# Kernel tuning notes

Hardware: AMD Instinct MI355X
Metric: run time of the kernel (lower is better)

## Reference

```python
import jax, jax.numpy as jnp
import numpy as np

B, SQ, SK, D, DV = 16, 2048, 2048, 128, 128
NUM_HEADS = 2
DROPOUT_P = 0.1
SCALE_FACTOR = 1.0 / (DROPOUT_P * NUM_HEADS)  # = 5.0; scores are divided by this


def setup_inputs() -> dict:
    key = jax.random.key(0)
    k1, k2, k3, k4 = jax.random.split(key, 4)
    x1 = jax.random.normal(k1, (B, SQ, D), dtype=jnp.float32)
    x2 = jax.random.normal(k2, (B, SK, D), dtype=jnp.float32)
    x3 = jax.random.normal(k3, (B, SK, DV), dtype=jnp.float32)
    # deterministic dropout keep-mask (True -> keep), keep prob = 1 - p
    drop_mask = jax.random.bernoulli(k4, 1.0 - DROPOUT_P, (B, SQ, SK))
    return {"x1": x1, "x2": x2, "x3": x3, "drop_mask": drop_mask}


def reference(x1, x2, x3, drop_mask):
    # v1 = x1 @ x2^T : [B, Sq, Sk]
    scores = jnp.einsum("bqd,bkd->bqk", x1, x2)
    # v2 = v1 / scale_factor (scale_factor = 1/(p*heads) = 5 -> multiply by 0.2)
    scores = scores * (1.0 / SCALE_FACTOR)
    probs = jax.nn.softmax(scores, axis=-1)
    # dropout with inverted scaling 1/(1-p)
    keep_scale = 1.0 / (1.0 - DROPOUT_P)
    probs = jnp.where(drop_mask, probs * keep_scale, 0.0)
    # output = probs @ x3 : [B, Sq, Dv]
    return jnp.einsum("bqk,bkv->bqv", probs, x3)
```

## Files before the change

kernel.cpp:

```cpp
#include <hip/hip_runtime.h>
#include <stdint.h>


#define B_   16
#define SQ_  2048
#define SK_  2048
#define D_   128
#define DV_  128
#define BK   64
#define NT   (SK_ / BK)

typedef short  s16x8 __attribute__((ext_vector_type(8)));
typedef float  f32x4 __attribute__((ext_vector_type(4)));
typedef unsigned int u32x4 __attribute__((ext_vector_type(4)));
typedef unsigned short u16;
typedef unsigned int   u32;

__device__ __forceinline__ u32 pk2(float a, float b) {
    u32 r;
    asm("v_cvt_pk_bf16_f32 %0, %1, %2" : "=v"(r) : "v"(a), "v"(b));
    return r;
}
__device__ __forceinline__ u16 f2bf(float f) { return (u16)pk2(f, 0.0f); }

__device__ __forceinline__ void gload16(u16* lds, const u16* g) {
    __builtin_amdgcn_global_load_lds((const __attribute__((address_space(1))) u32*)g,
                                     (__attribute__((address_space(3))) u32*)lds,
                                     16, 0, 0);
}

__global__ __launch_bounds__(256)
void prep_k(const float* __restrict__ Kg, u16* __restrict__ Kz)
{
    int g   = blockIdx.x * 256 + threadIdx.x;
    int b   = g >> 15;
    int rem = g & 32767;
    int k   = rem >> 4;
    int grp = rem & 15;
    const float* src = Kg + ((size_t)b * SK_ + k) * D_ + grp * 8;
    float4 x = *(const float4*)(src);
    float4 y = *(const float4*)(src + 4);
    u32x4 w = { pk2(x.x, x.y), pk2(x.z, x.w), pk2(y.x, y.y), pk2(y.z, y.w) };
    int c = (grp * 8) ^ ((k & 7) << 3);
    *(u32x4*)(&Kz[((size_t)b * SK_ + k) * D_ + c]) = w;
}

__global__ __launch_bounds__(256)
void prep_v(const float* __restrict__ Vg, u16* __restrict__ Vz)
{
    int g  = blockIdx.x * 256 + threadIdx.x;
    int kg = g & 7;
    int dv = (g >> 3) & 127;
    int kt = (g >> 10) & 31;
    int b  = g >> 15;
    const float* src = Vg + ((size_t)b * SK_ + kt * 64 + kg * 8) * DV_ + dv;
    float v[8];
    #pragma unroll
    for (int jj = 0; jj < 8; ++jj) v[jj] = src[(size_t)jj * DV_];
    u32x4 w = { pk2(v[0], v[1]), pk2(v[2], v[3]), pk2(v[4], v[5]), pk2(v[6], v[7]) };
    int c = (kg * 8) ^ ((dv & 7) << 3);
    *(u32x4*)(&Vz[(((size_t)b * 32 + kt) * 128 + dv) * 64 + c]) = w;
}

#define BODY(IT, MC, MN)                                                      \
  {                                                                           \
    __syncthreads();              \
    {                                                                         \
      const u16* Kt = Kz + kvbase + (size_t)(IT) * 8192;                      \
      const u16* Vt = Vz + kvbase + (size_t)(IT) * 8192;                      \
      _Pragma("unroll")                                                       \
      for (int i = 0; i < 4; ++i) {                                           \
        int c16 = (wave * 4 + i) * 512;                                       \
        gload16(&Ks[c16], &Kt[c16 + lane * 8]);                               \
        gload16(&Vs[c16], &Vt[c16 + lane * 8]);                               \
      }                                                                       \
    }                                                                         \
    __syncthreads();           \
    if ((IT) + 1 < NT) {                                                      \
      _Pragma("unroll")                                                       \
      for (int t = 0; t < 2; ++t)                                             \
        _Pragma("unroll")                                                     \
        for (int r = 0; r < 4; ++r)                                           \
          MN[t][r] = Mg[mbase + (size_t)r * SK_ + ((IT) + 1) * 64 + t * 16];  \
    }                                                                         \
    f32x4 s[2];                                                               \
    s[0] = (f32x4){0.f, 0.f, 0.f, 0.f};                                       \
    s[1] = (f32x4){0.f, 0.f, 0.f, 0.f};                                       \
    __builtin_amdgcn_s_setprio(1);                                            \
    _Pragma("unroll")                                                         \
    for (int kb = 0; kb < 4; ++kb) {                                          \
      _Pragma("unroll")                                                       \
      for (int t = 0; t < 2; ++t) {                                           \
        int kcol = kh * 32 + t * 16 + n16;                                    \
        int coff = (kb * 32 + quad * 8) ^ ((kcol & 7) << 3);                  \
        s16x8 bK = *(const s16x8*)(&Ks[kcol * 128 + coff]);                   \
        s[t] = __builtin_amdgcn_mfma_f32_16x16x32_bf16(aQ[kb], bK, s[t], 0, 0, 0); \
      }                                                                       \
    }                                                                         \
    __builtin_amdgcn_s_setprio(0);                                            \
    _Pragma("unroll")                                                         \
    for (int t = 0; t < 2; ++t)                                               \
      _Pragma("unroll")                                                       \
      for (int r = 0; r < 4; ++r) {                                           \
        float p = __expf(fmaf(s[t][r], 0.2f, -12.0f));                        \
        l_part[r] += p;                                   \
        float pv = MC[t][r] ? p : 0.f;                           \
        Ps[wave * 640 + (quad * 4 + r) * 40 + t * 16 + n16] = f2bf(pv);       \
      }                                                                       \
    s16x8 aP = *(const s16x8*)(&Ps[wave * 640 + n16 * 40 + quad * 8]);        \
    __builtin_amdgcn_s_setprio(1);                                            \
    _Pragma("unroll")                                                         \
    for (int nt = 0; nt < 8; ++nt) {                                          \
      int dv = nt * 16 + n16;                                                 \
      int coff = (kh * 32 + quad * 8) ^ ((dv & 7) << 3);                      \
      s16x8 bV = *(const s16x8*)(&Vs[dv * 64 + coff]);                        \
      o[nt] = __builtin_amdgcn_mfma_f32_16x16x32_bf16(aP, bV, o[nt], 0, 0, 0); \
    }                                                                         \
    __builtin_amdgcn_s_setprio(0);                                            \
  }

__global__ __launch_bounds__(256, 4)
void fattn_main(const float* __restrict__ Qg, const u16* __restrict__ Kz,
                const u16* __restrict__ Vz, const int* __restrict__ Mg,
                float* __restrict__ Og)
{
    __shared__ __align__(16) u16 Ks[64 * 128];
    __shared__ __align__(16) u16 Vs[128 * 64];
    __shared__ __align__(16) u16 Ps[4 * 16 * 40];
    __shared__ float lxch[32];

    const int tid  = threadIdx.x;
    const int wave = tid >> 6;
    const int lane = tid & 63;
    const int n16  = lane & 15;
    const int quad = lane >> 4;
    const int qh   = wave & 1;
    const int kh   = wave >> 1;

    const int raw = blockIdx.x;
    const int xcd = raw & 7;
    const int j   = raw >> 3;
    const int b   = xcd * 2 + (j & 1);
    const int q0  = (j >> 1) << 5;

    s16x8 aQ[4];
    {
        const float* qsrc = Qg + ((size_t)b * SQ_ + q0 + qh * 16 + n16) * D_;
        #pragma unroll
        for (int kb = 0; kb < 4; ++kb) {
            float4 x = *(const float4*)(qsrc + kb * 32 + quad * 8);
            float4 y = *(const float4*)(qsrc + kb * 32 + quad * 8 + 4);
            u32x4 w = { pk2(x.x, x.y), pk2(x.z, x.w), pk2(y.x, y.y), pk2(y.z, y.w) };
            aQ[kb] = __builtin_bit_cast(s16x8, w);
        }
    }

    f32x4 o[8];
    #pragma unroll
    for (int i = 0; i < 8; ++i) o[i] = (f32x4){0.f, 0.f, 0.f, 0.f};
    float l_part[4] = {0.f, 0.f, 0.f, 0.f};

    const size_t kvbase = (size_t)b * 262144;
    const size_t mbase  = ((size_t)b * SQ_ + q0 + qh * 16 + quad * 4) * (size_t)SK_
                        + kh * 32 + n16;

    int mA[2][4], mB[2][4];
    #pragma unroll
    for (int t = 0; t < 2; ++t)
        #pragma unroll
        for (int r = 0; r < 4; ++r)
            mA[t][r] = Mg[mbase + (size_t)r * SK_ + t * 16];

    for (int it = 0; it < NT; it += 2) {
        BODY(it,     mA, mB)
        BODY(it + 1, mB, mA)
    }

    float lr[4];
    #pragma unroll
    for (int r = 0; r < 4; ++r) {
        float l = l_part[r];
        #pragma unroll
        for (int off = 1; off < 16; off <<= 1) l += __shfl_xor(l, off);
        lr[r] = l;
    }
    __syncthreads();
    float* oxch = (float*)Ks;
    if (kh == 1) {
        #pragma unroll
        for (int r = 0; r < 4; ++r) {
            int row = qh * 16 + quad * 4 + r;
            #pragma unroll
            for (int nt = 0; nt < 8; ++nt)
                oxch[row * 128 + nt * 16 + n16] = o[nt][r];
            if (n16 == 0) lxch[row] = lr[r];
        }
    }
    __syncthreads();
    if (kh == 0) {
        const float ksc = 1.0f / 0.9f;
        #pragma unroll
        for (int r = 0; r < 4; ++r) {
            int row = qh * 16 + quad * 4 + r;
            float inv = ksc / (lr[r] + lxch[row]);
            size_t ob = ((size_t)b * SQ_ + q0 + row) * (size_t)DV_;
            #pragma unroll
            for (int nt = 0; nt < 8; ++nt)
                Og[ob + nt * 16 + n16] = (o[nt][r] + oxch[row * 128 + nt * 16 + n16]) * inv;
        }
    }
}

#define BQ_FB 64
#define LDQ  136
#define LDK  136
#define LDVT 72
#define LDP  72

__global__ __launch_bounds__(256, 2)
void fattn_fb(const float* __restrict__ Qg, const float* __restrict__ Kg,
              const float* __restrict__ Vg, const int* __restrict__ Mg,
              float* __restrict__ Og)
{
    __shared__ u16 Qs[BQ_FB * LDQ];
    __shared__ u16 Ks[BK * LDK];
    __shared__ u16 Vt[DV_ * LDVT];
    __shared__ u16 Ps[4 * 16 * LDP];

    const int tid  = threadIdx.x;
    const int wave = tid >> 6;
    const int lane = tid & 63;
    const int n16  = lane & 15;
    const int quad = lane >> 4;

    const int raw = blockIdx.x;
    const int xcd = raw & 7;
    const int j   = raw >> 3;
    const int b   = xcd * 2 + (j & 1);
    const int q0  = (j >> 1) << 6;

    const int srow = tid >> 4;
    const int scol = (tid & 15) * 8;
    const int vrot = (tid & 7) * 8;

    {
        const float* src = Qg + ((size_t)b * SQ_ + q0) * D_;
        #pragma unroll
        for (int c = 0; c < 4; ++c) {
            int row = c * 16 + srow;
            float4 v0 = *(const float4*)(&src[row * D_ + scol]);
            float4 v1 = *(const float4*)(&src[row * D_ + scol + 4]);
            uint4 pk = { pk2(v0.x, v0.y), pk2(v0.z, v0.w),
                         pk2(v1.x, v1.y), pk2(v1.z, v1.w) };
            *(uint4*)(&Qs[row * LDQ + scol]) = pk;
        }
    }
    __syncthreads();

    s16x8 aQ[4];
    {
        const int qr = wave * 16 + n16;
        #pragma unroll
        for (int kb = 0; kb < 4; ++kb)
            aQ[kb] = *(const s16x8*)(&Qs[qr * LDQ + kb * 32 + quad * 8]);
    }

    f32x4 o[8];
    #pragma unroll
    for (int i = 0; i < 8; ++i) o[i] = (f32x4){0.f, 0.f, 0.f, 0.f};
    float l_part[4] = {0.f, 0.f, 0.f, 0.f};

    const size_t mask_qbase = ((size_t)b * SQ_ + q0 + wave * 16 + quad * 4) * (size_t)SK_;
    const float* baseK = Kg + ((size_t)b * SK_) * D_;
    const float* baseV = Vg + ((size_t)b * SK_) * DV_;

    float4 kf[8], vf[8];
    #pragma unroll
    for (int c = 0; c < 4; ++c) {
        int row = c * 16 + srow;
        kf[2*c]   = *(const float4*)(&baseK[row * D_ + scol]);
        kf[2*c+1] = *(const float4*)(&baseK[row * D_ + scol + 4]);
        vf[2*c]   = *(const float4*)(&baseV[row * DV_ + scol]);
        vf[2*c+1] = *(const float4*)(&baseV[row * DV_ + scol + 4]);
    }
    int mkc[4][4], mkn[4][4];
    #pragma unroll
    for (int t = 0; t < 4; ++t)
        #pragma unroll
        for (int r = 0; r < 4; ++r)
            mkc[t][r] = Mg[mask_qbase + (size_t)r * SK_ + (t * 16 + n16)];

    for (int it = 0; it < NT; ++it) {
        __syncthreads();
        #pragma unroll
        for (int c = 0; c < 4; ++c) {
            int row = c * 16 + srow;
            uint4 pk = { pk2(kf[2*c].x, kf[2*c].y),     pk2(kf[2*c].z, kf[2*c].w),
                         pk2(kf[2*c+1].x, kf[2*c+1].y), pk2(kf[2*c+1].z, kf[2*c+1].w) };
            *(uint4*)(&Ks[row * LDK + scol]) = pk;
        }
        #pragma unroll
        for (int c = 0; c < 4; ++c) {
            int k    = c * 16 + srow;
            int rcol = (k + vrot) & 63;
            int dv0  = scol;
            u32 r0 = pk2(vf[2*c].x,   vf[2*c].y);
            u32 r1 = pk2(vf[2*c].z,   vf[2*c].w);
            u32 r2 = pk2(vf[2*c+1].x, vf[2*c+1].y);
            u32 r3 = pk2(vf[2*c+1].z, vf[2*c+1].w);
            Vt[(dv0 + 0) * LDVT + rcol] = (u16)r0;
            Vt[(dv0 + 1) * LDVT + rcol] = (u16)(r0 >> 16);
            Vt[(dv0 + 2) * LDVT + rcol] = (u16)r1;
            Vt[(dv0 + 3) * LDVT + rcol] = (u16)(r1 >> 16);
            Vt[(dv0 + 4) * LDVT + rcol] = (u16)r2;
            Vt[(dv0 + 5) * LDVT + rcol] = (u16)(r2 >> 16);
            Vt[(dv0 + 6) * LDVT + rcol] = (u16)r3;
            Vt[(dv0 + 7) * LDVT + rcol] = (u16)(r3 >> 16);
        }
        if (it + 1 < NT) {
            const int k0n = (it + 1) * BK;
            #pragma unroll
            for (int c = 0; c < 4; ++c) {
                int row = k0n + c * 16 + srow;
                kf[2*c]   = *(const float4*)(&baseK[row * D_ + scol]);
                kf[2*c+1] = *(const float4*)(&baseK[row * D_ + scol + 4]);
                vf[2*c]   = *(const float4*)(&baseV[row * DV_ + scol]);
                vf[2*c+1] = *(const float4*)(&baseV[row * DV_ + scol + 4]);
            }
            #pragma unroll
            for (int t = 0; t < 4; ++t)
                #pragma unroll
                for (int r = 0; r < 4; ++r)
                    mkn[t][r] = Mg[mask_qbase + (size_t)r * SK_ + (k0n + t * 16 + n16)];
        }
        __syncthreads();

        f32x4 s[4];
        #pragma unroll
        for (int t = 0; t < 4; ++t) s[t] = (f32x4){0.f, 0.f, 0.f, 0.f};
        #pragma unroll
        for (int kb = 0; kb < 4; ++kb) {
            #pragma unroll
            for (int t = 0; t < 4; ++t) {
                s16x8 bK = *(const s16x8*)(&Ks[(t * 16 + n16) * LDK + kb * 32 + quad * 8]);
                s[t] = __builtin_amdgcn_mfma_f32_16x16x32_bf16(aQ[kb], bK, s[t], 0, 0, 0);
            }
        }
        #pragma unroll
        for (int t = 0; t < 4; ++t)
            #pragma unroll
            for (int r = 0; r < 4; ++r) {
                float p = __expf(fmaf(s[t][r], 0.2f, -12.0f));
                l_part[r] += p;
                float pv = mkc[t][r] ? p : 0.f;
                Ps[(wave * 16 + quad * 4 + r) * LDP + t * 16 + n16] = f2bf(pv);
            }
        #pragma unroll
        for (int kk = 0; kk < 2; ++kk) {
            s16x8 aP = *(const s16x8*)(&Ps[(wave * 16 + n16) * LDP + kk * 32 + quad * 8]);
            #pragma unroll
            for (int nt = 0; nt < 8; ++nt) {
                int dv   = nt * 16 + n16;
                int rcol = (kk * 32 + quad * 8 + 8 * ((dv >> 3) & 7)) & 63;
                s16x8 bV = *(const s16x8*)(&Vt[dv * LDVT + rcol]);
                o[nt] = __builtin_amdgcn_mfma_f32_16x16x32_bf16(aP, bV, o[nt], 0, 0, 0);
            }
        }
        #pragma unroll
        for (int t = 0; t < 4; ++t)
            #pragma unroll
            for (int r = 0; r < 4; ++r) mkc[t][r] = mkn[t][r];
    }

    const float keep_scale = 1.0f / 0.9f;
    #pragma unroll
    for (int r = 0; r < 4; ++r) {
        float l = l_part[r];
        #pragma unroll
        for (int off = 1; off < 16; off <<= 1)
            l += __shfl_xor(l, off);
        float inv_l = keep_scale / l;
        size_t obase = ((size_t)b * SQ_ + q0 + wave * 16 + quad * 4 + r) * DV_;
        #pragma unroll
        for (int nt = 0; nt < 8; ++nt)
            Og[obase + nt * 16 + n16] = o[nt][r] * inv_l;
    }
}

extern "C" void kernel_launch(void* const* d_in, const int* in_sizes, int n_in,
                              void* d_out, int out_size, void* d_ws, size_t ws_size,
                              hipStream_t stream) {
    const float* Qg = (const float*)d_in[0];
    const float* Kg = (const float*)d_in[1];
    const float* Vg = (const float*)d_in[2];
    const int*   Mg = (const int*)d_in[3];
    float* Og = (float*)d_out;
    if (d_ws != nullptr && ws_size >= (size_t)16 * 1024 * 1024) {
        u16* Kz = (u16*)d_ws;
        u16* Vz = Kz + 4194304;
        prep_k<<<dim3(2048), 256, 0, stream>>>(Kg, Kz);
        prep_v<<<dim3(2048), 256, 0, stream>>>(Vg, Vz);
        fattn_main<<<dim3(1024), 256, 0, stream>>>(Qg, Kz, Vz, Mg, Og);
    } else {
        fattn_fb<<<dim3(512), 256, 0, stream>>>(Qg, Kg, Vg, Mg, Og);
    }
}
```

Baseline: 467.2 us.

## Pack dropout mask to bits in prep kernel and double-buffer K/V tiles

Adds a prep_m kernel that compresses the int32 dropout mask into one byte per thread per KV tile, laid out for the main kernel. The main kernel preloads its whole packed mask slice into LDS once, and double-buffers K/V tiles so the next tile's global-to-LDS load overlaps the current tile's compute, cutting one barrier per iteration. It also reorders the prep_v thread mapping for better coalescing. In exchange, LDS use roughly doubles, so occupancy drops (launch bounds go from 4 to 2 blocks per CU), and an extra pass reads the full int32 mask.

```diff
diff --git a/kernel.cpp b/kernel.cpp
--- a/kernel.cpp
+++ b/kernel.cpp
@@ -15,6 +15,7 @@
 typedef unsigned int u32x4 __attribute__((ext_vector_type(4)));
 typedef unsigned short u16;
 typedef unsigned int   u32;
+typedef unsigned char  u8;
 
 __device__ __forceinline__ u32 pk2(float a, float b) {
     u32 r;
@@ -23,7 +24,7 @@
 }
 __device__ __forceinline__ u16 f2bf(float f) { return (u16)pk2(f, 0.0f); }
 
-__device__ __forceinline__ void gload16(u16* lds, const u16* g) {
+__device__ __forceinline__ void gload16(void* lds, const void* g) {
     __builtin_amdgcn_global_load_lds((const __attribute__((address_space(1))) u32*)g,
                                      (__attribute__((address_space(3))) u32*)lds,
                                      16, 0, 0);
@@ -49,8 +50,8 @@
 void prep_v(const float* __restrict__ Vg, u16* __restrict__ Vz)
 {
     int g  = blockIdx.x * 256 + threadIdx.x;
-    int kg = g & 7;
-    int dv = (g >> 3) & 127;
+    int dv = g & 127;
+    int kg = (g >> 7) & 7;
     int kt = (g >> 10) & 31;
     int b  = g >> 15;
     const float* src = Vg + ((size_t)b * SK_ + kt * 64 + kg * 8) * DV_ + dv;
@@ -62,27 +63,49 @@
     *(u32x4*)(&Vz[(((size_t)b * 32 + kt) * 128 + dv) * 64 + c]) = w;
 }
 
-#define BODY(IT, MC, MN)                                                      \
+__global__ __launch_bounds__(256)
+void prep_m(const int* __restrict__ Mg, u8* __restrict__ Mp)
+{
+    const int bid  = blockIdx.x;
+    const int b    = bid >> 6;
+    const int qt   = bid & 63;
+    const int tid  = threadIdx.x;
+    const int wave = tid >> 6;
+    const int lane = tid & 63;
+    const int n16  = lane & 15;
+    const int quad = lane >> 4;
+    const int qh   = wave & 1;
+    const int kh   = wave >> 1;
+
+    const int* base = Mg + ((size_t)(b * SQ_ + qt * 32 + qh * 16 + quad * 4)) * SK_
+                    + kh * 32 + n16;
+    u8* out = Mp + (size_t)bid * 8192 + tid;
+
+    #pragma unroll 4
+    for (int kt = 0; kt < 32; ++kt) {
+        u32 m = 0;
+        #pragma unroll
+        for (int t = 0; t < 2; ++t)
+            #pragma unroll
+            for (int r = 0; r < 4; ++r)
+                m |= (base[(size_t)r * SK_ + kt * 64 + t * 16] != 0 ? 1u : 0u) << (t * 4 + r);
+        out[(size_t)kt * 256] = (u8)m;
+    }
+}
+
+#define STEP(IT, CUR, NXT)                                                    \
   {                                                                           \
-    __syncthreads();              \
-    {                                                                         \
-      const u16* Kt = Kz + kvbase + (size_t)(IT) * 8192;                      \
-      const u16* Vt = Vz + kvbase + (size_t)(IT) * 8192;                      \
+    if ((IT) + 1 < NT) {        \
+      const u16* Kt = Kz + kvbase + (size_t)((IT) + 1) * 8192;                \
+      const u16* Vt = Vz + kvbase + (size_t)((IT) + 1) * 8192;                \
       _Pragma("unroll")                                                       \
       for (int i = 0; i < 4; ++i) {                                           \
         int c16 = (wave * 4 + i) * 512;                                       \
-        gload16(&Ks[c16], &Kt[c16 + lane * 8]);                               \
-        gload16(&Vs[c16], &Vt[c16 + lane * 8]);                               \
+        gload16(&Kbuf[NXT][c16], &Kt[c16 + lane * 8]);                        \
+        gload16(&Vbuf[NXT][c16], &Vt[c16 + lane * 8]);                        \
       }                                                                       \
     }                                                                         \
-    __syncthreads();           \
-    if ((IT) + 1 < NT) {                                                      \
-      _Pragma("unroll")                                                       \
-      for (int t = 0; t < 2; ++t)                                             \
-        _Pragma("unroll")                                                     \
-        for (int r = 0; r < 4; ++r)                                           \
-          MN[t][r] = Mg[mbase + (size_t)r * SK_ + ((IT) + 1) * 64 + t * 16];  \
-    }                                                                         \
+    u32 mb = (u32)Ms[(IT) * 256 + tid];          \
     f32x4 s[2];                                                               \
     s[0] = (f32x4){0.f, 0.f, 0.f, 0.f};                                       \
     s[1] = (f32x4){0.f, 0.f, 0.f, 0.f};                                       \
@@ -93,7 +116,7 @@
       for (int t = 0; t < 2; ++t) {                                           \
         int kcol = kh * 32 + t * 16 + n16;                                    \
         int coff = (kb * 32 + quad * 8) ^ ((kcol & 7) << 3);                  \
-        s16x8 bK = *(const s16x8*)(&Ks[kcol * 128 + coff]);                   \
+        s16x8 bK = *(const s16x8*)(&Kbuf[CUR][kcol * 128 + coff]);            \
         s[t] = __builtin_amdgcn_mfma_f32_16x16x32_bf16(aQ[kb], bK, s[t], 0, 0, 0); \
       }                                                                       \
     }                                                                         \
@@ -104,7 +127,7 @@
       for (int r = 0; r < 4; ++r) {                                           \
         float p = __expf(fmaf(s[t][r], 0.2f, -12.0f));                        \
         l_part[r] += p;                                   \
-        float pv = MC[t][r] ? p : 0.f;                           \
+        float pv = ((mb >> (t * 4 + r)) & 1u) ? p : 0.f;                      \
         Ps[wave * 640 + (quad * 4 + r) * 40 + t * 16 + n16] = f2bf(pv);       \
       }                                                                       \
     s16x8 aP = *(const s16x8*)(&Ps[wave * 640 + n16 * 40 + quad * 8]);        \
@@ -113,20 +136,22 @@
     for (int nt = 0; nt < 8; ++nt) {                                          \
       int dv = nt * 16 + n16;                                                 \
       int coff = (kh * 32 + quad * 8) ^ ((dv & 7) << 3);                      \
-      s16x8 bV = *(const s16x8*)(&Vs[dv * 64 + coff]);                        \
+      s16x8 bV = *(const s16x8*)(&Vbuf[CUR][dv * 64 + coff]);                 \
       o[nt] = __builtin_amdgcn_mfma_f32_16x16x32_bf16(aP, bV, o[nt], 0, 0, 0); \
     }                                                                         \
     __builtin_amdgcn_s_setprio(0);                                            \
+    __syncthreads();    \
   }
 
-__global__ __launch_bounds__(256, 4)
+__global__ __launch_bounds__(256, 2)
 void fattn_main(const float* __restrict__ Qg, const u16* __restrict__ Kz,
-                const u16* __restrict__ Vz, const int* __restrict__ Mg,
+                const u16* __restrict__ Vz, const u8* __restrict__ Mp,
                 float* __restrict__ Og)
 {
-    __shared__ __align__(16) u16 Ks[64 * 128];
-    __shared__ __align__(16) u16 Vs[128 * 64];
+    __shared__ __align__(16) u16 Kbuf[2][64 * 128];
+    __shared__ __align__(16) u16 Vbuf[2][128 * 64];
     __shared__ __align__(16) u16 Ps[4 * 16 * 40];
+    __shared__ __align__(16) u8  Ms[32 * 256];
     __shared__ float lxch[32];
 
     const int tid  = threadIdx.x;
@@ -141,8 +166,25 @@
     const int xcd = raw & 7;
     const int j   = raw >> 3;
     const int b   = xcd * 2 + (j & 1);
-    const int q0  = (j >> 1) << 5;
-
+    const int qt  = j >> 1;
+    const int q0  = qt << 5;
+
+    {
+        const u8* Mpb = Mp + ((size_t)(b * 64 + qt)) * 8192;
+        #pragma unroll
+        for (int i = 0; i < 2; ++i) {
+            int off = (wave * 2 + i) * 1024;
+            gload16(&Ms[off], &Mpb[off + lane * 16]);
+        }
+        const u16* Kt = Kz + (size_t)b * 262144;
+        const u16* Vt = Vz + (size_t)b * 262144;
+        #pragma unroll
+        for (int i = 0; i < 4; ++i) {
+            int c16 = (wave * 4 + i) * 512;
+            gload16(&Kbuf[0][c16], &Kt[c16 + lane * 8]);
+            gload16(&Vbuf[0][c16], &Vt[c16 + lane * 8]);
+        }
+    }
     s16x8 aQ[4];
     {
         const float* qsrc = Qg + ((size_t)b * SQ_ + q0 + qh * 16 + n16) * D_;
@@ -161,19 +203,12 @@
     float l_part[4] = {0.f, 0.f, 0.f, 0.f};
 
     const size_t kvbase = (size_t)b * 262144;
-    const size_t mbase  = ((size_t)b * SQ_ + q0 + qh * 16 + quad * 4) * (size_t)SK_
-                        + kh * 32 + n16;
-
-    int mA[2][4], mB[2][4];
-    #pragma unroll
-    for (int t = 0; t < 2; ++t)
-        #pragma unroll
-        for (int r = 0; r < 4; ++r)
-            mA[t][r] = Mg[mbase + (size_t)r * SK_ + t * 16];
+
+    __syncthreads();
 
     for (int it = 0; it < NT; it += 2) {
-        BODY(it,     mA, mB)
-        BODY(it + 1, mB, mA)
+        STEP(it,     0, 1)
+        STEP(it + 1, 1, 0)
     }
 
     float lr[4];
@@ -184,8 +219,7 @@
         for (int off = 1; off < 16; off <<= 1) l += __shfl_xor(l, off);
         lr[r] = l;
     }
-    __syncthreads();
-    float* oxch = (float*)Ks;
+    float* oxch = (float*)Kbuf;
     if (kh == 1) {
         #pragma unroll
         for (int r = 0; r < 4; ++r) {
@@ -395,12 +429,14 @@
     const float* Vg = (const float*)d_in[2];
     const int*   Mg = (const int*)d_in[3];
     float* Og = (float*)d_out;
-    if (d_ws != nullptr && ws_size >= (size_t)16 * 1024 * 1024) {
+    if (d_ws != nullptr && ws_size >= (size_t)24 * 1024 * 1024) {
         u16* Kz = (u16*)d_ws;
         u16* Vz = Kz + 4194304;
+        u8*  Mp = (u8*)(Vz + 4194304);
         prep_k<<<dim3(2048), 256, 0, stream>>>(Kg, Kz);
         prep_v<<<dim3(2048), 256, 0, stream>>>(Vg, Vz);
-        fattn_main<<<dim3(1024), 256, 0, stream>>>(Qg, Kz, Vz, Mg, Og);
+        prep_m<<<dim3(1024), 256, 0, stream>>>(Mg, Mp);
+        fattn_main<<<dim3(1024), 256, 0, stream>>>(Qg, Kz, Vz, Mp, Og);
     } else {
         fattn_fb<<<dim3(512), 256, 0, stream>>>(Qg, Kg, Vg, Mg, Og);
     }
```

New measurement: 484.0 us. 1.04x slower.
